# Performance work log

Measured on AMD Instinct MI355X. Metric: run time of the kernel, lower is better.

The kernel has to match this reference:

```python
import math
import jax, jax.numpy as jnp
import numpy as np

B, A, U, S, E, HYP, H = 16384, 32, 64, 2048, 32, 64, 4
ATTEND_REG_COEF = 1e-3


def setup_inputs() -> dict:
    key = jax.random.key(0)
    ks = jax.random.split(key, 12)
    sc = 0.05
    return {
        "agent_qs": jax.random.normal(ks[0], (B, A), jnp.float32),
        "states": jax.random.normal(ks[1], (B, S), jnp.float32),
        # per-head selector hypernet: Linear(S,HYP)+ReLU+Linear(HYP,E,no bias)
        "sel_w1": jax.random.normal(ks[2], (H, S, HYP), jnp.float32) * sc,
        "sel_b1": jax.random.normal(ks[3], (H, HYP), jnp.float32) * sc,
        "sel_w2": jax.random.normal(ks[4], (H, HYP, E), jnp.float32) * sc,
        # per-head key extractor: Linear(U,E,no bias)
        "key_w": jax.random.normal(ks[5], (H, U, E), jnp.float32) * sc,
        # V net: Linear(S,E)+ReLU+Linear(E,1)
        "v_w1": jax.random.normal(ks[6], (S, E), jnp.float32) * sc,
        "v_b1": jax.random.normal(ks[7], (E,), jnp.float32) * sc,
        "v_w2": jax.random.normal(ks[8], (E, 1), jnp.float32) * sc,
        "v_b2": jax.random.normal(ks[9], (1,), jnp.float32) * sc,
    }


def reference(agent_qs, states, sel_w1, sel_b1, sel_w2, key_w, v_w1, v_b1, v_w2, v_b2):
    # nonlinear=False, weighted_head=False, state_bias=True (defaults used here)
    unit_states = states[:, : A * U].reshape(-1, A, U)  # [B, A, U]

    # per-head selectors: [B, H, E]
    h1 = jax.nn.relu(jnp.einsum("bs,hsk->bhk", states, sel_w1) + sel_b1[None])
    selectors = jnp.einsum("bhk,hke->bhe", h1, sel_w2)

    # per-head, per-agent keys: [B, H, A, E]
    keys = jnp.einsum("bau,hue->bhae", unit_states, key_w)

    # attention logits [B, H, A] (matches selector @ stacked-keys in torch)
    logits = jnp.einsum("bhe,bhae->bha", selectors, keys)
    weights = jax.nn.softmax(logits / math.sqrt(E), axis=-1)  # [B, H, A]

    head_attend = jnp.sum(weights, axis=1)  # [B, A]

    v = jax.nn.relu(states @ v_w1 + v_b1) @ v_w2 + v_b2  # [B, 1]

    # coef * sum over heads of mean(logits_h ** 2)
    attend_mag_regs = ATTEND_REG_COEF * jnp.sum(jnp.mean(logits ** 2, axis=(0, 2)))

    # per-head entropy: -(p * log(p + 1e-8)).sum(agents).mean(batch) -> [H]
    head_entropies = -jnp.mean(
        jnp.sum(weights * jnp.log(weights + 1e-8), axis=-1), axis=0
    )

    return head_attend, v, attend_mag_regs, head_entropies
```

## Files before the change

kernel.cpp:

```cpp
#include <hip/hip_runtime.h>
#include <hip/hip_bf16.h>

#define B_N 16384
#define A_N 32
#define U_N 64
#define S_N 2048
#define E_N 32
#define HYP_N 64
#define H_N 4
#define NREAL 288
#define NPADG 320

#define WS_WT    0
#define WS_MB    1310720
#define WS_PMAG  (WS_MB + 32768)
#define WS_PENT  (WS_PMAG + 65536)

#define OUT_V   (B_N * A_N)
#define OUT_MAG (OUT_V + B_N)
#define OUT_ENT (OUT_MAG + 1)

typedef __attribute__((ext_vector_type(8))) short bf16x8_t;
typedef __attribute__((ext_vector_type(4))) float floatx4_t;

__device__ __forceinline__ unsigned short f2b(float f) {
    union { float f; unsigned u; } v; v.f = f;
    unsigned r = v.u + 0x7FFFu + ((v.u >> 16) & 1u);
    return (unsigned short)(r >> 16);
}
__device__ __forceinline__ float b2f(unsigned x) {
    union { unsigned u; float f; } v; v.u = x << 16; return v.f;
}

__global__ __launch_bounds__(256) void pack_w_kernel(
        const float* __restrict__ sel_w1, const float* __restrict__ v_w1,
        const float* __restrict__ sel_w2, const float* __restrict__ key_w,
        unsigned short* __restrict__ Wt, unsigned short* __restrict__ Mb) {
    int idx = blockIdx.x * 256 + threadIdx.x;
    if (idx < NPADG * S_N) {
        int n = idx >> 11;
        int k = idx & 2047;
        float val = 0.0f;
        if (n < 256) {
            int h = n >> 6, kk = n & 63;
            val = sel_w1[((size_t)h * S_N + k) * HYP_N + kk];
        } else if (n < NREAL) {
            val = v_w1[(size_t)k * E_N + (n - 256)];
        }
        Wt[idx] = f2b(val);
    } else if (idx < NPADG * S_N + H_N * U_N * HYP_N) {
        int j = idx - NPADG * S_N;
        int h = j >> 12, u = (j >> 6) & 63, k = j & 63;
        const float* kw = key_w + ((size_t)h * U_N + u) * E_N;
        const float* w2 = sel_w2 + ((size_t)h * HYP_N + k) * E_N;
        float s = 0.0f;
#pragma unroll
        for (int e = 0; e < E_N; ++e) s = fmaf(kw[e], w2[e], s);
        Mb[j] = f2b(s);
    }
}

#define FM_BM 32
#define CHK 256
#define NCHK (S_N / CHK)
#define KSC (CHK / 32)
#define H1_STRIDE 312
#define TS_STRIDE 260

__global__ __launch_bounds__(256, 2) void fused_kernel(
        const float* __restrict__ states, const unsigned short* __restrict__ Wt,
        const float* __restrict__ sel_b1, const float* __restrict__ v_b1,
        const unsigned short* __restrict__ Mb,
        const float* __restrict__ v_w2, const float* __restrict__ v_b2,
        float* __restrict__ out, float* __restrict__ pmag, float* __restrict__ pent) {
    __shared__ __align__(16) char pool[53248];
    unsigned short* Abuf = (unsigned short*)pool;
    unsigned short* h1b  = (unsigned short*)pool;
    float*          tsb  = (float*)(pool + 19968);

    const int t = threadIdx.x;
    const int lane = t & 63;
    const int w = t >> 6;
    const int m0 = blockIdx.x * FM_BM;
    const int nw = w * 80;

    const int ar = t >> 3, aq = t & 7;
    const float* abase = states + (size_t)(m0 + ar) * S_N + aq * 32;

    floatx4_t acc[2][5] = {};
    float4 avn[8];
    bf16x8_t bq[2][5];
    const int bn15 = lane & 15, bko = (lane >> 4) * 8;

    auto loadA = [&](int ch) {
        const float* g = abase + ch * CHK;
#pragma unroll
        for (int i = 0; i < 8; ++i) avn[i] = ((const float4*)g)[i];
    };
    auto writeA = [&](unsigned short* dst) {
#pragma unroll
        for (int j = 0; j < 4; ++j) {
            int o = aq * 4 + j;
            int ph = (o & 24) | ((o & 7) ^ (ar & 7));
            uint4 u;
            u.x = (unsigned)f2b(avn[2*j].x)   | ((unsigned)f2b(avn[2*j].y)   << 16);
            u.y = (unsigned)f2b(avn[2*j].z)   | ((unsigned)f2b(avn[2*j].w)   << 16);
            u.z = (unsigned)f2b(avn[2*j+1].x) | ((unsigned)f2b(avn[2*j+1].y) << 16);
            u.w = (unsigned)f2b(avn[2*j+1].z) | ((unsigned)f2b(avn[2*j+1].w) << 16);
            *(uint4*)(dst + ar * 256 + ph * 8) = u;
        }
    };
    auto loadB = [&](bf16x8_t* q, int ksg) {
#pragma unroll
        for (int nt = 0; nt < 5; ++nt) {
            int n = nw + nt * 16 + bn15;
            q[nt] = *(const bf16x8_t*)(Wt + (size_t)n * S_N + ksg * 32 + bko);
        }
    };

    loadA(0);
    writeA(Abuf);
    loadA(1);
    loadB(bq[0], 0);
    loadB(bq[1], 1);
    __syncthreads();

#pragma unroll 1
    for (int chunk = 0; chunk < NCHK; ++chunk) {
        unsigned short* As = Abuf + (chunk & 1) * 8192;
        if (chunk < NCHK - 1) {
            writeA(Abuf + ((chunk & 1) ^ 1) * 8192);
            if (chunk < NCHK - 2) loadA(chunk + 2);
        }
#pragma unroll
        for (int ks = 0; ks < KSC; ++ks) {
            bf16x8_t af[2];
#pragma unroll
            for (int mt = 0; mt < 2; ++mt) {
                int r = mt * 16 + (lane & 15);
                int o = ks * 4 + (lane >> 4);
                int ph = (o & 24) | ((o & 7) ^ (r & 7));
                af[mt] = *(const bf16x8_t*)(As + r * 256 + ph * 8);
            }
#pragma unroll
            for (int nt = 0; nt < 5; ++nt) {
                acc[0][nt] = __builtin_amdgcn_mfma_f32_16x16x32_bf16(
                    af[0], bq[ks & 1][nt], acc[0][nt], 0, 0, 0);
                acc[1][nt] = __builtin_amdgcn_mfma_f32_16x16x32_bf16(
                    af[1], bq[ks & 1][nt], acc[1][nt], 0, 0, 0);
            }
            if (ks < KSC - 2 || chunk < NCHK - 1)
                loadB(bq[ks & 1], chunk * KSC + ks + 2);
        }
        __syncthreads();
    }

#pragma unroll
    for (int nt = 0; nt < 5; ++nt) {
        int n = nw + nt * 16 + (lane & 15);
        if (n >= NREAL) continue;
        float bias = (n < 256) ? sel_b1[n] : v_b1[n - 256];
        int slot = (n < 256) ? ((n >> 6) * 72 + (n & 63))
                             : (((n - 256) >> 3) * 72 + 64 + ((n - 256) & 7));
#pragma unroll
        for (int mt = 0; mt < 2; ++mt) {
#pragma unroll
            for (int rg = 0; rg < 4; ++rg) {
                int r = mt * 16 + (lane >> 4) * 4 + rg;
                float v = acc[mt][nt][rg] + bias;
                h1b[r * H1_STRIDE + slot] = f2b(v > 0.0f ? v : 0.0f);
            }
        }
    }
    __syncthreads();

    {
        const int h = w;
        floatx4_t tacc[2][4] = {};
#pragma unroll
        for (int s = 0; s < 2; ++s) {
            int k0 = s * 32 + (lane >> 4) * 8;
            bf16x8_t bfr[4];
#pragma unroll
            for (int ut = 0; ut < 4; ++ut) {
                int u = ut * 16 + (lane & 15);
                bfr[ut] = *(const bf16x8_t*)(Mb + ((size_t)(h * U_N + u) * 64) + k0);
            }
#pragma unroll
            for (int mt = 0; mt < 2; ++mt) {
                int r = mt * 16 + (lane & 15);
                bf16x8_t afr = *(const bf16x8_t*)(h1b + r * H1_STRIDE + h * 72 + k0);
#pragma unroll
                for (int ut = 0; ut < 4; ++ut)
                    tacc[mt][ut] = __builtin_amdgcn_mfma_f32_16x16x32_bf16(
                        afr, bfr[ut], tacc[mt][ut], 0, 0, 0);
            }
        }
#pragma unroll
        for (int mt = 0; mt < 2; ++mt)
#pragma unroll
            for (int ut = 0; ut < 4; ++ut)
#pragma unroll
                for (int rg = 0; rg < 4; ++rg) {
                    int r = mt * 16 + (lane >> 4) * 4 + rg;
                    int u = ut * 16 + (lane & 15);
                    tsb[r * TS_STRIDE + h * U_N + u] = tacc[mt][ut][rg];
                }
    }
    __syncthreads();

    const int a = lane & 31, uh = lane >> 5;
    float4 cur[8], nxt[8];
    {
        const float* up = states + (size_t)(m0 + w * 8) * S_N + a * 64 + uh * 32;
#pragma unroll
        for (int i = 0; i < 8; ++i) cur[i] = ((const float4*)up)[i];
    }
    for (int rr = 0; rr < 8; ++rr) {
        int r = w * 8 + rr;
        int b = m0 + r;
        if (rr < 7) {
            const float* up = states + (size_t)(b + 1) * S_N + a * 64 + uh * 32;
#pragma unroll
            for (int i = 0; i < 8; ++i) nxt[i] = ((const float4*)up)[i];
        }
        float pl[4];
#pragma unroll
        for (int h = 0; h < 4; ++h) {
            const float* tp = &tsb[r * TS_STRIDE + h * U_N + uh * 32];
            float s = 0.0f;
#pragma unroll
            for (int i = 0; i < 8; ++i) {
                float4 t4 = *(const float4*)(tp + i * 4);
                s = fmaf(cur[i].x, t4.x, s);
                s = fmaf(cur[i].y, t4.y, s);
                s = fmaf(cur[i].z, t4.z, s);
                s = fmaf(cur[i].w, t4.w, s);
            }
            pl[h] = s + __shfl_xor(s, 32, 64);
        }
        float mg = pl[0]*pl[0] + pl[1]*pl[1] + pl[2]*pl[2] + pl[3]*pl[3];
#pragma unroll
        for (int o = 16; o > 0; o >>= 1) mg += __shfl_xor(mg, o, 32);
        float hatt = 0.0f;
        float entv[4];
#pragma unroll
        for (int h = 0; h < 4; ++h) {
            float x = pl[h] * 0.17677669529663687f;
            float m = x;
#pragma unroll
            for (int o = 16; o > 0; o >>= 1) m = fmaxf(m, __shfl_xor(m, o, 32));
            float p = expf(x - m);
            float den = p;
#pragma unroll
            for (int o = 16; o > 0; o >>= 1) den += __shfl_xor(den, o, 32);
            float wv = p / den;
            hatt += wv;
            float e = wv * logf(wv + 1e-8f);
#pragma unroll
            for (int o = 16; o > 0; o >>= 1) e += __shfl_xor(e, o, 32);
            entv[h] = e;
        }
        if (uh == 0) {
            out[(size_t)b * A_N + a] = hatt;
            float pv = b2f((unsigned)h1b[r * H1_STRIDE + (a >> 3) * 72 + 64 + (a & 7)])
                       * v_w2[a];
#pragma unroll
            for (int o = 16; o > 0; o >>= 1) pv += __shfl_xor(pv, o, 32);
            if (a == 0) {
                out[OUT_V + b] = pv + v_b2[0];
                pmag[b] = mg;
#pragma unroll
                for (int h = 0; h < 4; ++h) pent[(size_t)h * B_N + b] = entv[h];
            }
        }
#pragma unroll
        for (int i = 0; i < 8; ++i) cur[i] = nxt[i];
    }
}

__global__ __launch_bounds__(256) void finalize_kernel(
        const float* __restrict__ pmag, const float* __restrict__ pent,
        float* __restrict__ out) {
    int which = blockIdx.x;
    const float* src = (which == 0) ? pmag : (pent + (size_t)(which - 1) * B_N);
    float s = 0.0f;
    for (int i = threadIdx.x; i < B_N; i += 256) s += src[i];
#pragma unroll
    for (int o = 32; o > 0; o >>= 1) s += __shfl_xor(s, o, 64);
    __shared__ float red[4];
    if ((threadIdx.x & 63) == 0) red[threadIdx.x >> 6] = s;
    __syncthreads();
    if (threadIdx.x == 0) {
        float tot = red[0] + red[1] + red[2] + red[3];
        if (which == 0) out[OUT_MAG] = 1e-3f * tot / (float)(B_N * A_N);
        else out[OUT_ENT + which - 1] = -tot / (float)B_N;
    }
}

extern "C" void kernel_launch(void* const* d_in, const int* in_sizes, int n_in,
                              void* d_out, int out_size, void* d_ws, size_t ws_size,
                              hipStream_t stream) {
    const float* states = (const float*)d_in[1];
    const float* sel_w1 = (const float*)d_in[2];
    const float* sel_b1 = (const float*)d_in[3];
    const float* sel_w2 = (const float*)d_in[4];
    const float* key_w  = (const float*)d_in[5];
    const float* v_w1   = (const float*)d_in[6];
    const float* v_b1   = (const float*)d_in[7];
    const float* v_w2   = (const float*)d_in[8];
    const float* v_b2   = (const float*)d_in[9];
    float* out = (float*)d_out;
    char* wsb  = (char*)d_ws;

    unsigned short* Wt  = (unsigned short*)(wsb + WS_WT);
    unsigned short* Mb  = (unsigned short*)(wsb + WS_MB);
    float* pmag         = (float*)(wsb + WS_PMAG);
    float* pent         = (float*)(wsb + WS_PENT);

    pack_w_kernel<<<dim3((NPADG * S_N + H_N * U_N * HYP_N + 255) / 256),
                    dim3(256), 0, stream>>>(sel_w1, v_w1, sel_w2, key_w, Wt, Mb);
    fused_kernel<<<dim3(B_N / FM_BM), dim3(256), 0, stream>>>(
        states, Wt, sel_b1, v_b1, Mb, v_w2, v_b2, out, pmag, pent);
    finalize_kernel<<<dim3(5), dim3(256), 0, stream>>>(pmag, pent, out);
}
```

Baseline: 332.6 us.

## Stage weight tiles in LDS via direct global-to-LDS DMA, double batch tile

Restructures the main projection GEMM. Each block now covers 64 batch rows with 512 threads. The shared weight tile is copied straight from global memory into swizzled, double-buffered LDS with global_load_lds, and every wave reads its B fragments from there. The states rows go directly into registers as A fragments, so the old LDS staging of A is gone. This cuts repeated L2/global reads of the packed weights per wave, but it uses much more LDS per block (~120KB), which likely limits the CU to one block and adds a barrier on every 64-wide K chunk.

```diff
diff --git a/kernel.cpp b/kernel.cpp
--- a/kernel.cpp
+++ b/kernel.cpp
@@ -22,6 +22,9 @@
 
 typedef __attribute__((ext_vector_type(8))) short bf16x8_t;
 typedef __attribute__((ext_vector_type(4))) float floatx4_t;
+
+#define AS1(p) ((const __attribute__((address_space(1))) void*)(p))
+#define AS3(p) ((__attribute__((address_space(3))) void*)(p))
 
 __device__ __forceinline__ unsigned short f2b(float f) {
     union { float f; unsigned u; } v; v.f = f;
@@ -60,122 +63,114 @@
     }
 }
 
-#define FM_BM 32
-#define CHK 256
-#define NCHK (S_N / CHK)
-#define KSC (CHK / 32)
+#define FM_BM 64
+#define NCHK 32
 #define H1_STRIDE 312
 #define TS_STRIDE 260
 
-__global__ __launch_bounds__(256, 2) void fused_kernel(
+__global__ __launch_bounds__(512, 2) void fused_kernel(
         const float* __restrict__ states, const unsigned short* __restrict__ Wt,
         const float* __restrict__ sel_b1, const float* __restrict__ v_b1,
         const unsigned short* __restrict__ Mb,
         const float* __restrict__ v_w2, const float* __restrict__ v_b2,
         float* __restrict__ out, float* __restrict__ pmag, float* __restrict__ pent) {
-    __shared__ __align__(16) char pool[53248];
-    unsigned short* Abuf = (unsigned short*)pool;
-    unsigned short* h1b  = (unsigned short*)pool;
-    float*          tsb  = (float*)(pool + 19968);
+    __shared__ __align__(16) char pool[81920 + 39936];
+    unsigned short* Bsm = (unsigned short*)pool;
+    unsigned short* h1b = (unsigned short*)(pool + 81920);
+    float*          tsb = (float*)pool;
 
     const int t = threadIdx.x;
     const int lane = t & 63;
     const int w = t >> 6;
     const int m0 = blockIdx.x * FM_BM;
-    const int nw = w * 80;
-
-    const int ar = t >> 3, aq = t & 7;
-    const float* abase = states + (size_t)(m0 + ar) * S_N + aq * 32;
-
-    floatx4_t acc[2][5] = {};
-    float4 avn[8];
-    bf16x8_t bq[2][5];
-    const int bn15 = lane & 15, bko = (lane >> 4) * 8;
-
-    auto loadA = [&](int ch) {
-        const float* g = abase + ch * CHK;
-#pragma unroll
-        for (int i = 0; i < 8; ++i) avn[i] = ((const float4*)g)[i];
+    const int g = w & 3;
+    const int nh = w >> 2;
+    const int nbase = nh * 160;
+
+    const float* arow = states + (size_t)(m0 + g * 16 + (lane & 15)) * S_N
+                        + ((lane >> 4) * 8);
+
+    floatx4_t acc[10] = {};
+    float4 av[2][2][2];
+
+    auto loadA = [&](int set, int chunk) {
+#pragma unroll
+        for (int s = 0; s < 2; ++s) {
+            const float* p = arow + chunk * 64 + s * 32;
+            av[set][s][0] = *(const float4*)p;
+            av[set][s][1] = *(const float4*)(p + 4);
+        }
     };
-    auto writeA = [&](unsigned short* dst) {
-#pragma unroll
-        for (int j = 0; j < 4; ++j) {
-            int o = aq * 4 + j;
-            int ph = (o & 24) | ((o & 7) ^ (ar & 7));
-            uint4 u;
-            u.x = (unsigned)f2b(avn[2*j].x)   | ((unsigned)f2b(avn[2*j].y)   << 16);
-            u.y = (unsigned)f2b(avn[2*j].z)   | ((unsigned)f2b(avn[2*j].w)   << 16);
-            u.z = (unsigned)f2b(avn[2*j+1].x) | ((unsigned)f2b(avn[2*j+1].y) << 16);
-            u.w = (unsigned)f2b(avn[2*j+1].z) | ((unsigned)f2b(avn[2*j+1].w) << 16);
-            *(uint4*)(dst + ar * 256 + ph * 8) = u;
+    auto dmaB = [&](int chunk) {
+        unsigned short* dst = Bsm + (chunk & 1) * 20480;
+        const int k0 = chunk * 64;
+#pragma unroll
+        for (int i = 0; i < 5; ++i) {
+            int p = i * 512 + t, n = p >> 3, sl = p & 7;
+            int cl = sl ^ (n & 7);
+            __builtin_amdgcn_global_load_lds(
+                AS1(Wt + (size_t)n * S_N + k0 + cl * 8),
+                AS3(dst + p * 8), 16, 0, 0);
         }
     };
-    auto loadB = [&](bf16x8_t* q, int ksg) {
-#pragma unroll
-        for (int nt = 0; nt < 5; ++nt) {
-            int n = nw + nt * 16 + bn15;
-            q[nt] = *(const bf16x8_t*)(Wt + (size_t)n * S_N + ksg * 32 + bko);
-        }
+    auto mkfrag = [&](int set, int s) -> bf16x8_t {
+        float4 x = av[set][s][0], y = av[set][s][1];
+        union { unsigned u[4]; bf16x8_t v; } r;
+        r.u[0] = (unsigned)f2b(x.x) | ((unsigned)f2b(x.y) << 16);
+        r.u[1] = (unsigned)f2b(x.z) | ((unsigned)f2b(x.w) << 16);
+        r.u[2] = (unsigned)f2b(y.x) | ((unsigned)f2b(y.y) << 16);
+        r.u[3] = (unsigned)f2b(y.z) | ((unsigned)f2b(y.w) << 16);
+        return r.v;
     };
 
-    loadA(0);
-    writeA(Abuf);
-    loadA(1);
-    loadB(bq[0], 0);
-    loadB(bq[1], 1);
+    loadA(0, 0);
+    loadA(1, 1);
+    dmaB(0);
+    dmaB(1);
     __syncthreads();
 
-#pragma unroll 1
-    for (int chunk = 0; chunk < NCHK; ++chunk) {
-        unsigned short* As = Abuf + (chunk & 1) * 8192;
-        if (chunk < NCHK - 1) {
-            writeA(Abuf + ((chunk & 1) ^ 1) * 8192);
-            if (chunk < NCHK - 2) loadA(chunk + 2);
-        }
-#pragma unroll
-        for (int ks = 0; ks < KSC; ++ks) {
-            bf16x8_t af[2];
-#pragma unroll
-            for (int mt = 0; mt < 2; ++mt) {
-                int r = mt * 16 + (lane & 15);
-                int o = ks * 4 + (lane >> 4);
-                int ph = (o & 24) | ((o & 7) ^ (r & 7));
-                af[mt] = *(const bf16x8_t*)(As + r * 256 + ph * 8);
-            }
-#pragma unroll
-            for (int nt = 0; nt < 5; ++nt) {
-                acc[0][nt] = __builtin_amdgcn_mfma_f32_16x16x32_bf16(
-                    af[0], bq[ks & 1][nt], acc[0][nt], 0, 0, 0);
-                acc[1][nt] = __builtin_amdgcn_mfma_f32_16x16x32_bf16(
-                    af[1], bq[ks & 1][nt], acc[1][nt], 0, 0, 0);
-            }
-            if (ks < KSC - 2 || chunk < NCHK - 1)
-                loadB(bq[ks & 1], chunk * KSC + ks + 2);
-        }
-        __syncthreads();
-    }
-
-#pragma unroll
-    for (int nt = 0; nt < 5; ++nt) {
-        int n = nw + nt * 16 + (lane & 15);
+    for (int c = 0; c < NCHK; ++c) {
+        const int set = c & 1;
+        bf16x8_t af0 = mkfrag(set, 0);
+        bf16x8_t af1 = mkfrag(set, 1);
+        if (c < NCHK - 2) loadA(set, c + 2);
+        if (c < NCHK - 1) dmaB(c + 1);
+        const unsigned short* Bs = Bsm + set * 20480;
+#pragma unroll
+        for (int s = 0; s < 2; ++s) {
+            bf16x8_t af = s ? af1 : af0;
+            const int cc = s * 4 + (lane >> 4);
+#pragma unroll
+            for (int nt = 0; nt < 10; ++nt) {
+                int n = nbase + nt * 16 + (lane & 15);
+                int ph = cc ^ (n & 7);
+                bf16x8_t bfr = *(const bf16x8_t*)(Bs + n * 64 + ph * 8);
+                acc[nt] = __builtin_amdgcn_mfma_f32_16x16x32_bf16(
+                    af, bfr, acc[nt], 0, 0, 0);
+            }
+        }
+        if (c < NCHK - 1) __syncthreads();
+    }
+
+#pragma unroll
+    for (int nt = 0; nt < 10; ++nt) {
+        int n = nbase + nt * 16 + (lane & 15);
         if (n >= NREAL) continue;
         float bias = (n < 256) ? sel_b1[n] : v_b1[n - 256];
         int slot = (n < 256) ? ((n >> 6) * 72 + (n & 63))
                              : (((n - 256) >> 3) * 72 + 64 + ((n - 256) & 7));
 #pragma unroll
-        for (int mt = 0; mt < 2; ++mt) {
-#pragma unroll
-            for (int rg = 0; rg < 4; ++rg) {
-                int r = mt * 16 + (lane >> 4) * 4 + rg;
-                float v = acc[mt][nt][rg] + bias;
-                h1b[r * H1_STRIDE + slot] = f2b(v > 0.0f ? v : 0.0f);
-            }
+        for (int rg = 0; rg < 4; ++rg) {
+            int r = g * 16 + (lane >> 4) * 4 + rg;
+            float v = acc[nt][rg] + bias;
+            h1b[r * H1_STRIDE + slot] = f2b(v > 0.0f ? v : 0.0f);
         }
     }
     __syncthreads();
 
     {
-        const int h = w;
+        const int h = w >> 1;
+        const int rb = (w & 1) * 32;
         floatx4_t tacc[2][4] = {};
 #pragma unroll
         for (int s = 0; s < 2; ++s) {
@@ -188,8 +183,8 @@
             }
 #pragma unroll
             for (int mt = 0; mt < 2; ++mt) {
-                int r = mt * 16 + (lane & 15);
-                bf16x8_t afr = *(const bf16x8_t*)(h1b + r * H1_STRIDE + h * 72 + k0);
+                bf16x8_t afr = *(const bf16x8_t*)(
+                    h1b + (rb + mt * 16 + (lane & 15)) * H1_STRIDE + h * 72 + k0);
 #pragma unroll
                 for (int ut = 0; ut < 4; ++ut)
                     tacc[mt][ut] = __builtin_amdgcn_mfma_f32_16x16x32_bf16(
@@ -202,7 +197,7 @@
             for (int ut = 0; ut < 4; ++ut)
 #pragma unroll
                 for (int rg = 0; rg < 4; ++rg) {
-                    int r = mt * 16 + (lane >> 4) * 4 + rg;
+                    int r = rb + mt * 16 + (lane >> 4) * 4 + rg;
                     int u = ut * 16 + (lane & 15);
                     tsb[r * TS_STRIDE + h * U_N + u] = tacc[mt][ut][rg];
                 }
@@ -320,7 +315,7 @@
 
     pack_w_kernel<<<dim3((NPADG * S_N + H_N * U_N * HYP_N + 255) / 256),
                     dim3(256), 0, stream>>>(sel_w1, v_w1, sel_w2, key_w, Wt, Mb);
-    fused_kernel<<<dim3(B_N / FM_BM), dim3(256), 0, stream>>>(
+    fused_kernel<<<dim3(B_N / FM_BM), dim3(512), 0, stream>>>(
         states, Wt, sel_b1, v_b1, Mb, v_w2, v_b2, out, pmag, pent);
     finalize_kernel<<<dim3(5), dim3(256), 0, stream>>>(pmag, pent, out);
 }
```

Measured after the change: 349.3 us. +5.0%, slower.
